# Performance work log

Measured on AMD Instinct MI355X. Metric: run time of the kernel, lower is better.

The kernel has to match this reference:

```python
import jax, jax.numpy as jnp
import numpy as np

B, NQ, NM, NHR, D, H, FF = 16, 100, 5440, 4096, 256, 8, 2048

def _ln(x, w, b):
    m = x.mean(-1, keepdims=True)
    v = ((x - m) ** 2).mean(-1, keepdims=True)
    return (x - m) * jax.lax.rsqrt(v + 1e-5) * w + b

def setup_inputs():
    key = jax.random.key(0)
    ks = iter(jax.random.split(key, 32))
    def rn(shape, s=1.0):
        return jax.random.normal(next(ks), shape, jnp.float32) * s
    return {
        'tgt': rn((B, NQ, D)),
        'memory': rn((B, NM, D)),
        'memory_hr': rn((B, NHR, D)),
        'prior_attn_bias': rn((B, NQ, NM)),
        'query_pos': rn((B, NQ, D)),
        'ln_cross_w': jnp.ones((D,)), 'ln_cross_b': jnp.zeros((D,)),
        'q_w': rn((D, D), 0.02), 'q_b': jnp.zeros((D,)),
        'k_w': rn((D, D), 0.02), 'k_b': jnp.zeros((D,)),
        'v_w': rn((D, D), 0.02), 'v_b': jnp.zeros((D,)),
        'out_w': rn((D, D), 0.02), 'out_b': jnp.zeros((D,)),
        'ln_self_w': jnp.ones((D,)), 'ln_self_b': jnp.zeros((D,)),
        'sa_in_w': rn((3 * D, D), 0.02), 'sa_in_b': jnp.zeros((3 * D,)),
        'sa_out_w': rn((D, D), 0.02), 'sa_out_b': jnp.zeros((D,)),
        'ln_ffn_w': jnp.ones((D,)), 'ln_ffn_b': jnp.zeros((D,)),
        'lin1_w': rn((FF, D), 0.02), 'lin1_b': jnp.zeros((FF,)),
        'lin2_w': rn((D, FF), 0.02), 'lin2_b': jnp.zeros((D,)),
        'me_w': rn((D, D), 0.02), 'me_b': jnp.zeros((D,)),
    }

def reference(tgt, memory, memory_hr, prior_attn_bias, query_pos,
              ln_cross_w, ln_cross_b, q_w, q_b, k_w, k_b, v_w, v_b,
              out_w, out_b, ln_self_w, ln_self_b, sa_in_w, sa_in_b,
              sa_out_w, sa_out_b, ln_ffn_w, ln_ffn_b, lin1_w, lin1_b,
              lin2_w, lin2_b, me_w, me_b):
    b, nq, d = tgt.shape
    nm = memory.shape[1]
    h = H
    dh = d // h
    scale = dh ** -0.5
    # ---- cross-attention with additive prior bias (eval mode: dropout = id) ----
    x = _ln(tgt, ln_cross_w, ln_cross_b)
    q = ((x + query_pos) @ q_w.T + q_b).reshape(b, nq, h, dh)
    k = (memory @ k_w.T + k_b).reshape(b, nm, h, dh)
    v = (memory @ v_w.T + v_b).reshape(b, nm, h, dh)
    attn = jnp.einsum('bqhd,bmhd->bhqm', q, k) * scale + prior_attn_bias[:, None]  # [b,h,nq,nm]
    a = jax.nn.softmax(attn, axis=-1)
    o = jnp.einsum('bhqm,bmhd->bqhd', a, v).reshape(b, nq, d)
    tgt = tgt + (o @ out_w.T + out_b)
    # ---- self-attention (torch nn.MultiheadAttention, batch_first, eval) ----
    z = _ln(tgt, ln_self_w, ln_self_b)
    zq = z + query_pos
    qs = (zq @ sa_in_w[:d].T + sa_in_b[:d]).reshape(b, nq, h, dh)
    ks = (zq @ sa_in_w[d:2 * d].T + sa_in_b[d:2 * d]).reshape(b, nq, h, dh)
    vs = (z @ sa_in_w[2 * d:].T + sa_in_b[2 * d:]).reshape(b, nq, h, dh)
    sattn = jax.nn.softmax(jnp.einsum('bqhd,bmhd->bhqm', qs, ks) * scale, axis=-1)
    so = jnp.einsum('bhqm,bmhd->bqhd', sattn, vs).reshape(b, nq, d)
    tgt = tgt + (so @ sa_out_w.T + sa_out_b)
    # ---- FFN ----
    y = _ln(tgt, ln_ffn_w, ln_ffn_b)
    y = jax.nn.gelu(y @ lin1_w.T + lin1_b, approximate=False) @ lin2_w.T + lin2_b
    tgt = tgt + y
    # ---- mask branch ----
    mask_logits = jnp.einsum('bqd,bmd->bqm', tgt @ me_w.T + me_b, memory_hr)
    return (tgt, mask_logits)
```

## Files before the change

kernel.cpp:

```cpp
#include <hip/hip_runtime.h>

typedef unsigned short u16;
typedef unsigned int u32;
typedef __bf16 bf16x8 __attribute__((ext_vector_type(8)));
typedef float f32x4 __attribute__((ext_vector_type(4)));
typedef float f32x16 __attribute__((ext_vector_type(16)));

#define NCH 17
#define NSTEP 10

__device__ __forceinline__ u16 f2b(float f) {
  u32 u = __float_as_uint(f);
  u32 r = (u + 0x7fffu + ((u >> 16) & 1u)) >> 16;
  return (u16)r;
}
__device__ __forceinline__ float b2f(u16 h) {
  return __uint_as_float(((u32)h) << 16);
}
__device__ __forceinline__ bf16x8 zero8() {
  union { uint4 u; bf16x8 v; } z; z.u = make_uint4(0u, 0u, 0u, 0u); return z.v;
}
__device__ __forceinline__ u32 cvtpk(float lo, float hi) {
  u32 r;
  asm("v_cvt_pk_bf16_f32 %0, %1, %2" : "=v"(r) : "v"(lo), "v"(hi));
  return r;
}

struct Seg { const float* in; u16* out; int n4; };
struct PrepArgs {
  Seg seg[7];
  const float *k_w, *v_w, *k_b, *v_b, *pbias;
  u16 *Wf;
  uint4 *biasT5;
  float *kvB;
};

__global__ __launch_bounds__(256)
void prep_kernel(PrepArgs a)
{
  __shared__ float S[100][34];
  const int bx = blockIdx.x, tid = threadIdx.x;
  if (bx < 1472) {
    int bxr = bx;
#pragma unroll
    for (int k = 0; k < 7; ++k) {
      const int nb = a.seg[k].n4 >> 8;
      if (bxr < nb) {
        const int i = bxr * 256 + tid;
        const float4 f = *(const float4*)(a.seg[k].in + (size_t)i * 4);
        uint2 pk; pk.x = cvtpk(f.x, f.y); pk.y = cvtpk(f.z, f.w);
        *(uint2*)(a.seg[k].out + (size_t)i * 4) = pk;
        return;
      }
      bxr -= nb;
    }
    return;
  } else if (bx < 1536) {
    const int i = bx - 1472, gI = i >> 3, ks = i & 7;
    const int nt = tid >> 6, lane = tid & 63, lr = lane & 15, g = lane >> 4;
    const float* src = (gI < 4 ? a.k_w + (size_t)(gI * 64 + nt * 16 + lr) * 256
                               : a.v_w + (size_t)((gI - 4) * 64 + nt * 16 + lr) * 256)
                       + ks * 32 + g * 8;
    const float4 f0 = *(const float4*)src;
    const float4 f1 = *(const float4*)(src + 4);
    uint4 pk;
    pk.x = cvtpk(f0.x, f0.y); pk.y = cvtpk(f0.z, f0.w);
    pk.z = cvtpk(f1.x, f1.y); pk.w = cvtpk(f1.z, f1.w);
    *(uint4*)(a.Wf + (size_t)((gI * 8 + ks) * 4 + nt) * 512 + lane * 8) = pk;
  } else if (bx < 1538) {
    const int i = (bx - 1536) * 256 + tid;
    a.kvB[i] = (i < 256) ? a.k_b[i] : a.v_b[i - 256];
  } else {
    const int bt = bx - 1538;
    const int b = bt / 170, sg = bt - b * 170;
    const int m0 = sg * 32;
    for (int idx = tid; idx < 800; idx += 256) {
      const int q = idx >> 3, seg = idx & 7;
      const float4 v = *(const float4*)(a.pbias + (size_t)(b * 100 + q) * 5440 + m0 + seg * 4);
      S[q][seg * 4 + 0] = v.x; S[q][seg * 4 + 1] = v.y;
      S[q][seg * 4 + 2] = v.z; S[q][seg * 4 + 3] = v.w;
    }
    __syncthreads();
#pragma unroll
    for (int pass = 0; pass < 2; ++pass) {
      const int idx = pass * 256 + tid;
      const int qb = idx >> 7, r2 = idx & 127;
      const int half = r2 >> 6, lane = r2 & 63;
      const int q = qb * 32 + (lane & 31), hh = lane >> 5;
      u16 hv[8];
#pragma unroll
      for (int i = 0; i < 8; ++i) {
        const int reg = half * 8 + i;
        const int m = (reg & 3) + 8 * (reg >> 2) + 4 * hh;
        hv[i] = (q < 100) ? f2b(S[q][m]) : (u16)0;
      }
      uint4 pk;
      pk.x = (u32)hv[0] | ((u32)hv[1] << 16);
      pk.y = (u32)hv[2] | ((u32)hv[3] << 16);
      pk.z = (u32)hv[4] | ((u32)hv[5] << 16);
      pk.w = (u32)hv[6] | ((u32)hv[7] << 16);
      a.biasT5[((size_t)(bt * 4 + qb)) * 128 + half * 64 + lane] = pk;
    }
  }
}

template<int ROWS>
__device__ __forceinline__ void ln_stage(const float* __restrict__ x, int row0,
    const float* __restrict__ w, const float* __restrict__ b,
    const float* __restrict__ pos, u16* As)
{
  const int tid = threadIdx.x, lane = tid & 63, wid = tid >> 6;
  const float4 wv = *(const float4*)(w + lane * 4);
  const float4 bv = *(const float4*)(b + lane * 4);
#pragma unroll
  for (int rr = 0; rr < ROWS / 4; ++rr) {
    const int rl = wid * (ROWS / 4) + rr;
    const size_t o = (size_t)(row0 + rl) * 256 + lane * 4;
    const float4 v = *(const float4*)(x + o);
    float s = v.x + v.y + v.z + v.w;
#pragma unroll
    for (int m = 1; m < 64; m <<= 1) s += __shfl_xor(s, m);
    const float mean = s * (1.f / 256.f);
    const float d0 = v.x - mean, d1 = v.y - mean, d2 = v.z - mean, d3 = v.w - mean;
    float ss = d0 * d0 + d1 * d1 + d2 * d2 + d3 * d3;
#pragma unroll
    for (int m = 1; m < 64; m <<= 1) ss += __shfl_xor(ss, m);
    const float rs = rsqrtf(ss * (1.f / 256.f) + 1e-5f);
    float y0 = d0 * rs * wv.x + bv.x;
    float y1 = d1 * rs * wv.y + bv.y;
    float y2 = d2 * rs * wv.z + bv.z;
    float y3 = d3 * rs * wv.w + bv.w;
    if (pos) {
      const float4 pv = *(const float4*)(pos + o);
      y0 += pv.x; y1 += pv.y; y2 += pv.z; y3 += pv.w;
    }
    uint2 pk; pk.x = cvtpk(y0, y1); pk.y = cvtpk(y2, y3);
    const int byte = (rl * 512 + lane * 8) ^ ((rl & 7) << 4);
    *(uint2*)((char*)As + byte) = pk;
  }
}

__device__ __forceinline__ void gemm16x128(const u16* As, const u16* __restrict__ W,
                                           u16 (*Ws)[40], f32x4 acc[2])
{
  const int tid = threadIdx.x, lane = tid & 63, wid = tid >> 6;
  const int g = lane >> 4, lr = lane & 15;
  for (int k0 = 0; k0 < 256; k0 += 32) {
    for (int cid = tid; cid < 512; cid += 256) {
      const int r = cid >> 2, cg = (cid & 3) * 8;
      *(uint4*)&Ws[r][cg] = *(const uint4*)(W + (size_t)r * 256 + k0 + cg);
    }
    __syncthreads();
    const int abyte = (lr * 512 + k0 * 2 + g * 16) ^ ((lr & 7) << 4);
    const bf16x8 af = *(const bf16x8*)((const char*)As + abyte);
#pragma unroll
    for (int nt = 0; nt < 2; ++nt) {
      const bf16x8 bfr = *(const bf16x8*)&Ws[wid * 32 + nt * 16 + lr][g * 8];
      acc[nt] = __builtin_amdgcn_mfma_f32_16x16x32_bf16(af, bfr, acc[nt], 0, 0, 0);
    }
    __syncthreads();
  }
}

__global__ __launch_bounds__(256)
void qproj_kernel(const float* __restrict__ x, const float* __restrict__ lnw,
                  const float* __restrict__ lnb, const float* __restrict__ pos,
                  const u16* __restrict__ W, const float* __restrict__ bias,
                  u16* __restrict__ out, float scale)
{
  __shared__ u16 As[16 * 256];
  __shared__ u16 Ws[128][40];
  const int tid = threadIdx.x, lane = tid & 63, wid = tid >> 6;
  const int g = lane >> 4, lr = lane & 15;
  const int row0 = blockIdx.x * 16, n0 = blockIdx.y * 128;
  ln_stage<16>(x, row0, lnw, lnb, pos, As);
  f32x4 acc[2] = {};
  gemm16x128(As, W + (size_t)n0 * 256, Ws, acc);
#pragma unroll
  for (int nt = 0; nt < 2; ++nt) {
    const int col = n0 + wid * 32 + nt * 16 + lr;
    const float bv = bias[col];
#pragma unroll
    for (int r = 0; r < 4; ++r) {
      const int row = row0 + g * 4 + r;
      out[(size_t)row * 256 + col] = f2b((acc[nt][r] + bv) * scale);
    }
  }
}

__global__ __launch_bounds__(256)
void sain_kernel(const float* __restrict__ x, const float* __restrict__ lnw,
                 const float* __restrict__ lnb, const float* __restrict__ pos,
                 const u16* __restrict__ W, const float* __restrict__ bias,
                 float* __restrict__ qkb, float* __restrict__ vsb)
{
  __shared__ u16 As[16 * 256];
  __shared__ u16 Ws[128][40];
  const int tid = threadIdx.x, lane = tid & 63, wid = tid >> 6;
  const int g = lane >> 4, lr = lane & 15;
  const int row0 = blockIdx.x * 16, y = blockIdx.y;
  ln_stage<16>(x, row0, lnw, lnb, (y < 4) ? pos : nullptr, As);
  f32x4 acc[2] = {};
  gemm16x128(As, W + (size_t)y * 128 * 256, Ws, acc);
#pragma unroll
  for (int nt = 0; nt < 2; ++nt) {
    const int cl = wid * 32 + nt * 16 + lr;
    const float bv = bias[y * 128 + cl];
#pragma unroll
    for (int r = 0; r < 4; ++r) {
      const int row = row0 + g * 4 + r;
      const float v = acc[nt][r] + bv;
      if (y < 4) qkb[(size_t)row * 512 + y * 128 + cl] = v;
      else       vsb[(size_t)row * 256 + (y - 4) * 128 + cl] = v;
    }
  }
}

__global__ __launch_bounds__(256)
void ffn1_kernel(const float* __restrict__ x, const float* __restrict__ lnw,
                 const float* __restrict__ lnb, const u16* __restrict__ W,
                 const float* __restrict__ bias, u16* __restrict__ out)
{
  __shared__ u16 As[64 * 256];
  __shared__ u16 Ws[256][40];
  const int tid = threadIdx.x, lane = tid & 63, wid = tid >> 6;
  const int g = lane >> 4, lr = lane & 15;
  const int row0 = blockIdx.x * 64, n0 = blockIdx.y * 256;
  ln_stage<64>(x, row0, lnw, lnb, nullptr, As);
  f32x4 acc[16] = {};
  for (int k0 = 0; k0 < 256; k0 += 32) {
    for (int cid = tid; cid < 1024; cid += 256) {
      const int r = cid >> 2, cg = (cid & 3) * 8;
      *(uint4*)&Ws[r][cg] = *(const uint4*)(W + (size_t)(n0 + r) * 256 + k0 + cg);
    }
    __syncthreads();
    const int arow = wid * 16 + lr;
    const int abyte = (arow * 512 + k0 * 2 + g * 16) ^ ((arow & 7) << 4);
    const bf16x8 af = *(const bf16x8*)((const char*)As + abyte);
#pragma unroll
    for (int nt = 0; nt < 16; ++nt) {
      const bf16x8 bfr = *(const bf16x8*)&Ws[nt * 16 + lr][g * 8];
      acc[nt] = __builtin_amdgcn_mfma_f32_16x16x32_bf16(af, bfr, acc[nt], 0, 0, 0);
    }
    __syncthreads();
  }
#pragma unroll
  for (int nt = 0; nt < 16; ++nt) {
    const int col = n0 + nt * 16 + lr;
    const float bv = bias[col];
#pragma unroll
    for (int r = 0; r < 4; ++r) {
      const int row = row0 + wid * 16 + g * 4 + r;
      float v = acc[nt][r] + bv;
      v = 0.5f * v * (1.f + erff(v * 0.70710678118654752f));
      out[(size_t)row * 2048 + col] = f2b(v);
    }
  }
}

template<int BM, int BN, int WM, int WN, int GELU_, int RES_, int OF32, int OBF>
__global__ __launch_bounds__(256)
void gemm_kernel(const u16* __restrict__ Ap, const u16* __restrict__ W,
                 const float* __restrict__ bias, const float* __restrict__ res,
                 float* __restrict__ Cf, u16* __restrict__ Cb,
                 int M, int N, int K, float scale)
{
  constexpr int WROWS = BM / WM;
  constexpr int WCOLS = BN / WN;
  constexpr int MT = WROWS / 16;
  constexpr int NT = WCOLS / 16;
  static_assert(WM * WN == 4, "4 waves");
  __shared__ u16 As[BM][40];
  __shared__ u16 Ws[BN][40];
  const int tid = threadIdx.x, lane = tid & 63, wid = tid >> 6;
  const int g = lane >> 4, lr = lane & 15;
  const int m0 = blockIdx.x * BM, n0 = blockIdx.y * BN;
  const int wm = wid / WN, wn = wid % WN;
  f32x4 acc[MT][NT] = {};
  for (int k0 = 0; k0 < K; k0 += 32) {
    for (int cid = tid; cid < BM * 4; cid += 256) {
      int r = cid >> 2, cg = (cid & 3) * 8;
      *(uint4*)&As[r][cg] = *(const uint4*)(Ap + (size_t)(m0 + r) * K + k0 + cg);
    }
    for (int cid = tid; cid < BN * 4; cid += 256) {
      int r = cid >> 2, cg = (cid & 3) * 8;
      *(uint4*)&Ws[r][cg] = *(const uint4*)(W + (size_t)(n0 + r) * K + k0 + cg);
    }
    __syncthreads();
    bf16x8 af[MT], bfr[NT];
#pragma unroll
    for (int mt = 0; mt < MT; ++mt) af[mt] = *(const bf16x8*)&As[wm * WROWS + mt * 16 + lr][g * 8];
#pragma unroll
    for (int nt = 0; nt < NT; ++nt) bfr[nt] = *(const bf16x8*)&Ws[wn * WCOLS + nt * 16 + lr][g * 8];
#pragma unroll
    for (int mt = 0; mt < MT; ++mt)
#pragma unroll
      for (int nt = 0; nt < NT; ++nt)
        acc[mt][nt] = __builtin_amdgcn_mfma_f32_16x16x32_bf16(af[mt], bfr[nt], acc[mt][nt], 0, 0, 0);
    __syncthreads();
  }
#pragma unroll
  for (int mt = 0; mt < MT; ++mt)
#pragma unroll
    for (int nt = 0; nt < NT; ++nt) {
      const int col = n0 + wn * WCOLS + nt * 16 + lr;
      const float bv = bias[col];
#pragma unroll
      for (int r = 0; r < 4; ++r) {
        const int row = m0 + wm * WROWS + mt * 16 + g * 4 + r;
        float v = (acc[mt][nt][r] + bv) * scale;
        if constexpr (GELU_) v = 0.5f * v * (1.f + erff(v * 0.70710678118654752f));
        if constexpr (RES_) v += res[(size_t)row * N + col];
        if constexpr (OF32) Cf[(size_t)row * N + col] = v;
        if constexpr (OBF) Cb[(size_t)row * N + col] = f2b(v);
      }
    }
}

__global__ __launch_bounds__(512, 4)
void kv_gemm_kernel(const float* __restrict__ A, const u16* __restrict__ Wf,
                    const float* __restrict__ biasKV,
                    u16* __restrict__ Kb, u16* __restrict__ Vt)
{
  __shared__ u16 As[64 * 256];
  __shared__ u16 Vs[256 * 64];
  const int tid = threadIdx.x, lane = tid & 63, wid = tid >> 6;
  const int g = lane >> 4, lr = lane & 15;
  const int bidx = blockIdx.x / 85, t = blockIdx.x - bidx * 85;
  const int row0 = blockIdx.x * 64;

  for (int ch = tid; ch < 2048; ch += 512) {
    const int r = ch >> 5, c8 = (ch & 31) * 8;
    const float* ap = A + (size_t)(row0 + r) * 256 + c8;
    const float4 f0 = *(const float4*)ap;
    const float4 f1 = *(const float4*)(ap + 4);
    uint4 pk;
    pk.x = cvtpk(f0.x, f0.y);
    pk.y = cvtpk(f0.z, f0.w);
    pk.z = cvtpk(f1.x, f1.y);
    pk.w = cvtpk(f1.z, f1.w);
    const int byte = r * 512 + c8 * 2;
    *(uint4*)((char*)As + (byte ^ ((r & 7) << 4))) = pk;
  }
  __syncthreads();

  const u16* wbase = Wf + (size_t)wid * 8 * 4 * 512 + lane * 8;
  f32x4 acc[4][4] = {};
#pragma unroll 2
  for (int ks = 0; ks < 8; ++ks) {
    bf16x8 bfv[4], af[4];
#pragma unroll
    for (int nt = 0; nt < 4; ++nt)
      bfv[nt] = *(const bf16x8*)(wbase + (ks * 4 + nt) * 512);
#pragma unroll
    for (int mt = 0; mt < 4; ++mt) {
      const int r = mt * 16 + lr;
      const int byte = r * 512 + ks * 64 + g * 16;
      af[mt] = *(const bf16x8*)((const char*)As + (byte ^ ((r & 7) << 4)));
    }
#pragma unroll
    for (int mt = 0; mt < 4; ++mt)
#pragma unroll
      for (int nt = 0; nt < 4; ++nt)
        acc[mt][nt] = __builtin_amdgcn_mfma_f32_16x16x32_bf16(af[mt], bfv[nt], acc[mt][nt], 0, 0, 0);
  }

  const int isV = wid >> 2;
  if (isV) {
#pragma unroll
    for (int nt = 0; nt < 4; ++nt) {
      const int col = (wid - 4) * 64 + nt * 16 + lr;
      const float bv = biasKV[256 + col];
#pragma unroll
      for (int mt = 0; mt < 4; ++mt) {
        const int slot = (mt >> 1) * 32 + 16 * (mt & 1) + 8 * (g & 1) + 4 * (g >> 1);
#pragma unroll
        for (int r = 0; r < 4; r += 2) {
          const u32 val = cvtpk(acc[mt][nt][r] + bv, acc[mt][nt][r + 1] + bv);
          const int byte = (col * 128 + (slot + r) * 2) ^ ((col & 7) << 4);
          *(u32*)((char*)Vs + byte) = val;
        }
      }
    }
  }
  __syncthreads();

  if (!isV) {
#pragma unroll
    for (int nt = 0; nt < 4; ++nt) {
      const int col = wid * 64 + nt * 16 + lr;
      const float bv = biasKV[col];
#pragma unroll
      for (int mt = 0; mt < 4; ++mt)
#pragma unroll
        for (int r = 0; r < 4; r += 2) {
          const u32 pk = cvtpk(acc[mt][nt][r] + bv, acc[mt][nt][r + 1] + bv);
          const int rowA = mt * 16 + g * 4 + r;
          const int rowB = rowA + 1;
          *(u16*)((char*)As + ((rowA * 512 + col * 2) ^ ((rowA & 7) << 4))) = (u16)pk;
          *(u16*)((char*)As + ((rowB * 512 + col * 2) ^ ((rowB & 7) << 4))) = (u16)(pk >> 16);
        }
    }
  } else {
    const size_t vbase = (size_t)bidx * 256 * 5440 + (size_t)t * 64;
    const int t2 = tid - 256;
#pragma unroll
    for (int p = 0; p < 8; ++p) {
      const int idx = p * 256 + t2;
      const int col = idx >> 3, chunk = idx & 7;
      const int lbyte = col * 128 + ((chunk * 16) ^ ((col & 7) << 4));
      const uint4 v = *(const uint4*)((const char*)Vs + lbyte);
      *(uint4*)(Vt + vbase + (size_t)col * 5440 + chunk * 8) = v;
    }
  }
  __syncthreads();
#pragma unroll
  for (int p = 0; p < 4; ++p) {
    const int idx = p * 512 + tid;
    const int row = idx >> 5, c16 = idx & 31;
    const int lbyte = row * 512 + ((c16 * 16) ^ ((row & 7) << 4));
    const uint4 v = *(const uint4*)((const char*)As + lbyte);
    *(uint4*)(Kb + (size_t)(row0 + row) * 256 + c16 * 8) = v;
  }
}

__global__ __launch_bounds__(256, 3)
void cross_attn_kernel(const u16* __restrict__ Q, const u16* __restrict__ Kb,
                       const u16* __restrict__ Vt, const uint4* __restrict__ biasT5,
                       u32* __restrict__ Opp, float* __restrict__ ML)
{
  const int tid = threadIdx.x, lane = tid & 63, wid = tid >> 6;
  const int ql = lane & 31, hh = lane >> 5;
  const int b = blockIdx.y, c = blockIdx.x;
  const int head = blockIdx.z * 4 + wid;
  const int m_base = c * (5440 / NCH);

  bf16x8 qf[4][2];
#pragma unroll
  for (int qb = 0; qb < 4; ++qb) {
    const int q = qb * 32 + ql;
#pragma unroll
    for (int hf = 0; hf < 2; ++hf)
      qf[qb][hf] = (q < 100)
        ? *(const bf16x8*)&Q[(size_t)(b * 100 + q) * 256 + head * 32 + hf * 16 + hh * 8]
        : zero8();
  }
  float M[4], L[4];
  f32x16 O[4];
#pragma unroll
  for (int qb = 0; qb < 4; ++qb) {
    M[qb] = -1e30f; L[qb] = 0.f;
#pragma unroll
    for (int i = 0; i < 16; ++i) O[qb][i] = 0.f;
  }

  for (int s = 0; s < NSTEP; ++s) {
    const int m0 = m_base + s * 32;
    const u16* kp = &Kb[(size_t)(b * 5440 + m0 + ql) * 256 + head * 32 + hh * 8];
    const bf16x8 kf0 = *(const bf16x8*)kp;
    const bf16x8 kf1 = *(const bf16x8*)(kp + 16);
    const u16* vp = &Vt[((size_t)(b * 8 + head) * 32 + ql) * 5440 + m0 + hh * 8];
    const bf16x8 vf0 = *(const bf16x8*)vp;
    const bf16x8 vf1 = *(const bf16x8*)(vp + 16);
    const uint4* bb = biasT5 + ((size_t)(b * 170 + c * NSTEP + s) * 4) * 128 + lane;
#pragma unroll
    for (int qb = 0; qb < 4; ++qb) {
      const uint4 b0 = bb[qb * 128];
      const uint4 b1 = bb[qb * 128 + 64];
      f32x16 Sv = {};
      __builtin_amdgcn_s_setprio(1);
      Sv = __builtin_amdgcn_mfma_f32_32x32x16_bf16(kf0, qf[qb][0], Sv, 0, 0, 0);
      Sv = __builtin_amdgcn_mfma_f32_32x32x16_bf16(kf1, qf[qb][1], Sv, 0, 0, 0);
      __builtin_amdgcn_s_setprio(0);
      const u32 bw[8] = {b0.x, b0.y, b0.z, b0.w, b1.x, b1.y, b1.z, b1.w};
#pragma unroll
      for (int i = 0; i < 8; ++i) {
        Sv[2 * i]     += b2f((u16)bw[i]);
        Sv[2 * i + 1] += b2f((u16)(bw[i] >> 16));
      }
      float t8[8];
#pragma unroll
      for (int i = 0; i < 8; ++i) t8[i] = fmaxf(Sv[2 * i], Sv[2 * i + 1]);
      float t4a = fmaxf(fmaxf(t8[0], t8[1]), fmaxf(t8[2], t8[3]));
      float t4b = fmaxf(fmaxf(t8[4], t8[5]), fmaxf(t8[6], t8[7]));
      float mx = fmaxf(t4a, t4b);
      mx = fmaxf(mx, __shfl_xor(mx, 32));
      const float newM = fmaxf(M[qb], mx);
      const float al = __expf(M[qb] - newM);
      M[qb] = newM;
      float p[16];
#pragma unroll
      for (int i = 0; i < 16; ++i) p[i] = __expf(Sv[i] - newM);
      float s8[8];
#pragma unroll
      for (int i = 0; i < 8; ++i) s8[i] = p[2 * i] + p[2 * i + 1];
      const float sum = ((s8[0] + s8[1]) + (s8[2] + s8[3])) + ((s8[4] + s8[5]) + (s8[6] + s8[7]));
      L[qb] = L[qb] * al + sum;
#pragma unroll
      for (int i = 0; i < 16; ++i) O[qb][i] *= al;
      union { uint4 u; bf16x8 v; } pb0, pb1;
      pb0.u.x = cvtpk(p[0], p[1]);   pb0.u.y = cvtpk(p[2], p[3]);
      pb0.u.z = cvtpk(p[4], p[5]);   pb0.u.w = cvtpk(p[6], p[7]);
      pb1.u.x = cvtpk(p[8], p[9]);   pb1.u.y = cvtpk(p[10], p[11]);
      pb1.u.z = cvtpk(p[12], p[13]); pb1.u.w = cvtpk(p[14], p[15]);
      __builtin_amdgcn_s_setprio(1);
      O[qb] = __builtin_amdgcn_mfma_f32_32x32x16_bf16(vf0, pb0.v, O[qb], 0, 0, 0);
      O[qb] = __builtin_amdgcn_mfma_f32_32x32x16_bf16(vf1, pb1.v, O[qb], 0, 0, 0);
      __builtin_amdgcn_s_setprio(0);
    }
  }
  const int bh = b * 8 + head;
#pragma unroll
  for (int qb = 0; qb < 4; ++qb) {
    const int q = qb * 32 + ql;
    const float Lt = L[qb] + __shfl_xor(L[qb], 32);
    if (q < 100) {
      const size_t rb = (size_t)(bh * NCH + c) * 128 + q;
#pragma unroll
      for (int i = 0; i < 8; ++i)
        Opp[rb * 16 + hh * 8 + i] = cvtpk(O[qb][2 * i], O[qb][2 * i + 1]);
      if (hh == 0) { ML[rb * 2] = M[qb]; ML[rb * 2 + 1] = Lt; }
    }
  }
}

__global__ __launch_bounds__(256)
void reduce_attn_kernel(const u32* __restrict__ Opp, const float* __restrict__ ML,
                        u16* __restrict__ outb)
{
  const int row = blockIdx.x;
  const int b = row / 100, q = row % 100;
  const int h = threadIdx.x >> 5, d = threadIdx.x & 31;
  const int bh = b * 8 + h;
  const int reg = (d & 3) + 4 * (d >> 3);
  const int slot = ((d >> 2) & 1) * 8 + (reg >> 1);
  const int half = reg & 1;
  float gm = -1e30f;
  for (int c = 0; c < NCH; ++c) gm = fmaxf(gm, ML[((size_t)(bh * NCH + c) * 128 + q) * 2]);
  float l = 0.f, o = 0.f;
  for (int c = 0; c < NCH; ++c) {
    const size_t rb = (size_t)(bh * NCH + c) * 128 + q;
    const float w = __expf(ML[rb * 2] - gm);
    l += ML[rb * 2 + 1] * w;
    const u32 pv = Opp[rb * 16 + slot];
    o += b2f((u16)(half ? (pv >> 16) : pv)) * w;
  }
  outb[(size_t)row * 256 + h * 32 + d] = f2b(o / l);
}

__global__ __launch_bounds__(128)
void self_attn_kernel(const float* __restrict__ qk, const float* __restrict__ vs,
                      u16* __restrict__ so)
{
  __shared__ u16 kk[100][36];
  __shared__ u16 vv[100][36];
  __shared__ float S[100][101];
  const int b = blockIdx.x >> 3, h = blockIdx.x & 7;
  const int t = threadIdx.x;
  for (int e = t; e < 3200; e += 128) {
    const int r = e >> 5, cq = e & 31;
    kk[r][cq] = f2b(qk[(size_t)(b * 100 + r) * 512 + 256 + h * 32 + cq]);
    vv[r][cq] = f2b(vs[(size_t)(b * 100 + r) * 256 + h * 32 + cq]);
  }
  __syncthreads();
  if (t < 100) {
    float qr_[32];
#pragma unroll
    for (int cq = 0; cq < 32; ++cq) qr_[cq] = qk[(size_t)(b * 100 + t) * 512 + h * 32 + cq];
    for (int m = 0; m < 100; ++m) {
      float dp = 0.f;
#pragma unroll
      for (int cq = 0; cq < 32; ++cq) dp += qr_[cq] * b2f(kk[m][cq]);
      S[t][m] = dp * 0.17677669529663687f;
    }
    float mx = -1e30f;
    for (int m = 0; m < 100; ++m) mx = fmaxf(mx, S[t][m]);
    float sum = 0.f;
    for (int m = 0; m < 100; ++m) { const float p = __expf(S[t][m] - mx); S[t][m] = p; sum += p; }
    const float inv = 1.f / sum;
    float o[32];
#pragma unroll
    for (int cq = 0; cq < 32; ++cq) o[cq] = 0.f;
    for (int m = 0; m < 100; ++m) {
      const float p = S[t][m];
#pragma unroll
      for (int cq = 0; cq < 32; ++cq) o[cq] += p * b2f(vv[m][cq]);
    }
#pragma unroll
    for (int cq = 0; cq < 32; ++cq)
      so[(size_t)(b * 100 + t) * 256 + h * 32 + cq] = f2b(o[cq] * inv);
  }
}

__global__ __launch_bounds__(256)
void mask_gemm_kernel(const u16* __restrict__ tm, const float* __restrict__ hr,
                      float* __restrict__ out)
{
  __shared__ u16 As[112][40];
  __shared__ u16 Bs[64][40];
  const int tid = threadIdx.x, lane = tid & 63, wid = tid >> 6;
  const int g = lane >> 4, lr = lane & 15;
  const int b = blockIdx.y, n0 = blockIdx.x * 64;
  f32x4 acc[7] = {};
  for (int k0 = 0; k0 < 256; k0 += 32) {
    for (int cid = tid; cid < 448; cid += 256) {
      const int r = cid >> 2, cg = (cid & 3) * 8;
      uint4 val = {0u, 0u, 0u, 0u};
      if (r < 100) val = *(const uint4*)&tm[(size_t)(b * 100 + r) * 256 + k0 + cg];
      *(uint4*)&As[r][cg] = val;
    }
    {
      const int r = tid >> 2, cg = (tid & 3) * 8;
      const float* hp = hr + (size_t)(b * 4096 + n0 + r) * 256 + k0 + cg;
      float4 f0 = *(const float4*)hp;
      float4 f1 = *(const float4*)(hp + 4);
      uint4 pk;
      pk.x = cvtpk(f0.x, f0.y); pk.y = cvtpk(f0.z, f0.w);
      pk.z = cvtpk(f1.x, f1.y); pk.w = cvtpk(f1.z, f1.w);
      *(uint4*)&Bs[r][cg] = pk;
    }
    __syncthreads();
    const bf16x8 bfr = *(const bf16x8*)&Bs[wid * 16 + lr][g * 8];
#pragma unroll
    for (int mt = 0; mt < 7; ++mt) {
      const bf16x8 af = *(const bf16x8*)&As[mt * 16 + lr][g * 8];
      acc[mt] = __builtin_amdgcn_mfma_f32_16x16x32_bf16(af, bfr, acc[mt], 0, 0, 0);
    }
    __syncthreads();
  }
#pragma unroll
  for (int mt = 0; mt < 7; ++mt)
#pragma unroll
    for (int r = 0; r < 4; ++r) {
      const int qr = mt * 16 + g * 4 + r;
      if (qr < 100)
        out[(size_t)(b * 100 + qr) * 4096 + n0 + wid * 16 + lr] = acc[mt][r];
    }
}

extern "C" void kernel_launch(void* const* d_in, const int* in_sizes, int n_in,
                              void* d_out, int out_size, void* d_ws, size_t ws_size,
                              hipStream_t stream)
{
  (void)in_sizes; (void)n_in; (void)out_size; (void)ws_size;
  const float* tgt      = (const float*)d_in[0];
  const float* memory   = (const float*)d_in[1];
  const float* memhr    = (const float*)d_in[2];
  const float* pbias    = (const float*)d_in[3];
  const float* qpos     = (const float*)d_in[4];
  const float* lncw     = (const float*)d_in[5];
  const float* lncb     = (const float*)d_in[6];
  const float* q_w      = (const float*)d_in[7];
  const float* q_b      = (const float*)d_in[8];
  const float* k_w      = (const float*)d_in[9];
  const float* k_b      = (const float*)d_in[10];
  const float* v_w      = (const float*)d_in[11];
  const float* v_b      = (const float*)d_in[12];
  const float* out_w    = (const float*)d_in[13];
  const float* out_b    = (const float*)d_in[14];
  const float* lnsw     = (const float*)d_in[15];
  const float* lnsb     = (const float*)d_in[16];
  const float* sa_in_w  = (const float*)d_in[17];
  const float* sa_in_b  = (const float*)d_in[18];
  const float* sa_out_w = (const float*)d_in[19];
  const float* sa_out_b = (const float*)d_in[20];
  const float* lnfw     = (const float*)d_in[21];
  const float* lnfb     = (const float*)d_in[22];
  const float* l1w      = (const float*)d_in[23];
  const float* l1b      = (const float*)d_in[24];
  const float* l2w      = (const float*)d_in[25];
  const float* l2b      = (const float*)d_in[26];
  const float* me_w     = (const float*)d_in[27];
  const float* me_b     = (const float*)d_in[28];
  float* outf = (float*)d_out;

  char* ws = (char*)d_ws;
  size_t off = 0;
  auto alloc = [&](size_t bytes) -> void* {
    void* p = ws + off;
    off = (off + bytes + 255) & ~(size_t)255;
    return p;
  };
  u16*   Wf    = (u16*)alloc((size_t)131072 * 2);
  u16*   qW    = (u16*)alloc((size_t)65536 * 2);
  u16*   outW  = (u16*)alloc((size_t)65536 * 2);
  u16*   saW   = (u16*)alloc((size_t)196608 * 2);
  u16*   saoW  = (u16*)alloc((size_t)65536 * 2);
  u16*   l1W   = (u16*)alloc((size_t)524288 * 2);
  u16*   l2W   = (u16*)alloc((size_t)524288 * 2);
  u16*   meW   = (u16*)alloc((size_t)65536 * 2);
  float* kvB   = (float*)alloc((size_t)512 * 4);
  uint4* biasT5= (uint4*)alloc((size_t)16 * 170 * 4 * 128 * 16);
  u16*   Qb    = (u16*)alloc((size_t)409600 * 2);
  u16*   Kb    = (u16*)alloc((size_t)22282240 * 2);
  u16*   Vt    = (u16*)alloc((size_t)22282240 * 2);
  u32*   Opp   = (u32*)alloc((size_t)(128 * NCH * 128 * 16) * 4);
  float* MLp   = (float*)alloc((size_t)(128 * NCH * 128 * 2) * 4);
  u16*   attno = (u16*)alloc((size_t)409600 * 2);
  float* tgt1  = (float*)alloc((size_t)409600 * 4);
  float* qkb   = (float*)alloc((size_t)819200 * 4);
  float* vsb   = (float*)alloc((size_t)409600 * 4);
  u16*   sob   = (u16*)alloc((size_t)409600 * 2);
  float* tgt2  = (float*)alloc((size_t)409600 * 4);
  u16*   hb    = (u16*)alloc((size_t)3276800 * 2);
  u16*   t3b   = (u16*)alloc((size_t)409600 * 2);
  u16*   tmb   = (u16*)alloc((size_t)409600 * 2);

  const float SCALE = 0.17677669529663687f;

  PrepArgs pa;
  pa.seg[0] = {q_w,      qW,   16384};
  pa.seg[1] = {out_w,    outW, 16384};
  pa.seg[2] = {sa_in_w,  saW,  49152};
  pa.seg[3] = {sa_out_w, saoW, 16384};
  pa.seg[4] = {l1w,      l1W,  131072};
  pa.seg[5] = {l2w,      l2W,  131072};
  pa.seg[6] = {me_w,     meW,  16384};
  pa.k_w = k_w; pa.v_w = v_w; pa.k_b = k_b; pa.v_b = v_b; pa.pbias = pbias;
  pa.Wf = Wf; pa.biasT5 = biasT5; pa.kvB = kvB;
  prep_kernel<<<4258, 256, 0, stream>>>(pa);

  qproj_kernel<<<dim3(100, 2), 256, 0, stream>>>(tgt, lncw, lncb, qpos, qW, q_b, Qb, SCALE);
  kv_gemm_kernel<<<dim3(1360), 512, 0, stream>>>(memory, Wf, kvB, Kb, Vt);
  cross_attn_kernel<<<dim3(NCH, 16, 2), 256, 0, stream>>>(Qb, Kb, Vt, biasT5, Opp, MLp);
  reduce_attn_kernel<<<1600, 256, 0, stream>>>(Opp, MLp, attno);
  gemm_kernel<16, 128, 1, 4, 0, 1, 1, 0><<<dim3(100, 2), 256, 0, stream>>>(
      attno, outW, out_b, tgt, tgt1, nullptr, 1600, 256, 256, 1.f);

  sain_kernel<<<dim3(100, 6), 256, 0, stream>>>(tgt1, lnsw, lnsb, qpos, saW, sa_in_b, qkb, vsb);
  self_attn_kernel<<<128, 128, 0, stream>>>(qkb, vsb, sob);
  gemm_kernel<16, 128, 1, 4, 0, 1, 1, 0><<<dim3(100, 2), 256, 0, stream>>>(
      sob, saoW, sa_out_b, tgt1, tgt2, nullptr, 1600, 256, 256, 1.f);

  ffn1_kernel<<<dim3(25, 8), 256, 0, stream>>>(tgt2, lnfw, lnfb, l1W, l1b, hb);
  gemm_kernel<16, 128, 1, 4, 0, 1, 1, 1><<<dim3(100, 2), 256, 0, stream>>>(
      hb, l2W, l2b, tgt2, outf, t3b, 1600, 256, 2048, 1.f);

  gemm_kernel<16, 128, 1, 4, 0, 0, 0, 1><<<dim3(100, 2), 256, 0, stream>>>(
      t3b, meW, me_b, nullptr, nullptr, tmb, 1600, 256, 256, 1.f);
  mask_gemm_kernel<<<dim3(64, 16), 256, 0, stream>>>(tmb, memhr, outf + 409600);
}
```

Measured before the change: 326.5 us.

## Remap cross-attention waves to query blocks of one head

Each wave of the cross-attention kernel now owns a single 32-query block of one head, instead of one head with all four query blocks. The grid grows from 2 to 8 in z, so there are four times as many blocks and each thread keeps far fewer registers (one O accumulator instead of four). Launch bounds rise to 4 blocks per SIMD-level occupancy target. The cost is that K and V fragments are now loaded once per query block rather than shared across four, which multiplies global/L2 traffic for K/V, and the wave holding queries 96-127 does mostly padding work.

Result: faster. 312.7 us (-4.2%).

```diff
diff --git a/kernel.cpp b/kernel.cpp
--- a/kernel.cpp
+++ b/kernel.cpp
@@ -424,35 +424,28 @@
   }
 }
 
-__global__ __launch_bounds__(256, 3)
+__global__ __launch_bounds__(256, 4)
 void cross_attn_kernel(const u16* __restrict__ Q, const u16* __restrict__ Kb,
                        const u16* __restrict__ Vt, const uint4* __restrict__ biasT5,
                        u32* __restrict__ Opp, float* __restrict__ ML)
 {
-  const int tid = threadIdx.x, lane = tid & 63, wid = tid >> 6;
+  const int tid = threadIdx.x, lane = tid & 63, qb = tid >> 6;
   const int ql = lane & 31, hh = lane >> 5;
   const int b = blockIdx.y, c = blockIdx.x;
-  const int head = blockIdx.z * 4 + wid;
+  const int head = blockIdx.z;
   const int m_base = c * (5440 / NCH);
-
-  bf16x8 qf[4][2];
-#pragma unroll
-  for (int qb = 0; qb < 4; ++qb) {
-    const int q = qb * 32 + ql;
-#pragma unroll
-    for (int hf = 0; hf < 2; ++hf)
-      qf[qb][hf] = (q < 100)
-        ? *(const bf16x8*)&Q[(size_t)(b * 100 + q) * 256 + head * 32 + hf * 16 + hh * 8]
-        : zero8();
-  }
-  float M[4], L[4];
-  f32x16 O[4];
-#pragma unroll
-  for (int qb = 0; qb < 4; ++qb) {
-    M[qb] = -1e30f; L[qb] = 0.f;
-#pragma unroll
-    for (int i = 0; i < 16; ++i) O[qb][i] = 0.f;
-  }
+  const int q = qb * 32 + ql;
+
+  bf16x8 qf0 = zero8(), qf1 = zero8();
+  if (q < 100) {
+    const u16* qp = &Q[(size_t)(b * 100 + q) * 256 + head * 32 + hh * 8];
+    qf0 = *(const bf16x8*)qp;
+    qf1 = *(const bf16x8*)(qp + 16);
+  }
+  float M = -1e30f, L = 0.f;
+  f32x16 O;
+#pragma unroll
+  for (int i = 0; i < 16; ++i) O[i] = 0.f;
 
   for (int s = 0; s < NSTEP; ++s) {
     const int m0 = m_base + s * 32;
@@ -462,65 +455,58 @@
     const u16* vp = &Vt[((size_t)(b * 8 + head) * 32 + ql) * 5440 + m0 + hh * 8];
     const bf16x8 vf0 = *(const bf16x8*)vp;
     const bf16x8 vf1 = *(const bf16x8*)(vp + 16);
-    const uint4* bb = biasT5 + ((size_t)(b * 170 + c * NSTEP + s) * 4) * 128 + lane;
-#pragma unroll
-    for (int qb = 0; qb < 4; ++qb) {
-      const uint4 b0 = bb[qb * 128];
-      const uint4 b1 = bb[qb * 128 + 64];
-      f32x16 Sv = {};
-      __builtin_amdgcn_s_setprio(1);
-      Sv = __builtin_amdgcn_mfma_f32_32x32x16_bf16(kf0, qf[qb][0], Sv, 0, 0, 0);
-      Sv = __builtin_amdgcn_mfma_f32_32x32x16_bf16(kf1, qf[qb][1], Sv, 0, 0, 0);
-      __builtin_amdgcn_s_setprio(0);
-      const u32 bw[8] = {b0.x, b0.y, b0.z, b0.w, b1.x, b1.y, b1.z, b1.w};
-#pragma unroll
-      for (int i = 0; i < 8; ++i) {
-        Sv[2 * i]     += b2f((u16)bw[i]);
-        Sv[2 * i + 1] += b2f((u16)(bw[i] >> 16));
-      }
-      float t8[8];
-#pragma unroll
-      for (int i = 0; i < 8; ++i) t8[i] = fmaxf(Sv[2 * i], Sv[2 * i + 1]);
-      float t4a = fmaxf(fmaxf(t8[0], t8[1]), fmaxf(t8[2], t8[3]));
-      float t4b = fmaxf(fmaxf(t8[4], t8[5]), fmaxf(t8[6], t8[7]));
-      float mx = fmaxf(t4a, t4b);
-      mx = fmaxf(mx, __shfl_xor(mx, 32));
-      const float newM = fmaxf(M[qb], mx);
-      const float al = __expf(M[qb] - newM);
-      M[qb] = newM;
-      float p[16];
-#pragma unroll
-      for (int i = 0; i < 16; ++i) p[i] = __expf(Sv[i] - newM);
-      float s8[8];
-#pragma unroll
-      for (int i = 0; i < 8; ++i) s8[i] = p[2 * i] + p[2 * i + 1];
-      const float sum = ((s8[0] + s8[1]) + (s8[2] + s8[3])) + ((s8[4] + s8[5]) + (s8[6] + s8[7]));
-      L[qb] = L[qb] * al + sum;
-#pragma unroll
-      for (int i = 0; i < 16; ++i) O[qb][i] *= al;
-      union { uint4 u; bf16x8 v; } pb0, pb1;
-      pb0.u.x = cvtpk(p[0], p[1]);   pb0.u.y = cvtpk(p[2], p[3]);
-      pb0.u.z = cvtpk(p[4], p[5]);   pb0.u.w = cvtpk(p[6], p[7]);
-      pb1.u.x = cvtpk(p[8], p[9]);   pb1.u.y = cvtpk(p[10], p[11]);
-      pb1.u.z = cvtpk(p[12], p[13]); pb1.u.w = cvtpk(p[14], p[15]);
-      __builtin_amdgcn_s_setprio(1);
-      O[qb] = __builtin_amdgcn_mfma_f32_32x32x16_bf16(vf0, pb0.v, O[qb], 0, 0, 0);
-      O[qb] = __builtin_amdgcn_mfma_f32_32x32x16_bf16(vf1, pb1.v, O[qb], 0, 0, 0);
-      __builtin_amdgcn_s_setprio(0);
-    }
+    const uint4* bb = biasT5 + ((size_t)((b * 170 + c * NSTEP + s) * 4 + qb)) * 128 + lane;
+    const uint4 b0 = bb[0];
+    const uint4 b1 = bb[64];
+    f32x16 Sv = {};
+    __builtin_amdgcn_s_setprio(1);
+    Sv = __builtin_amdgcn_mfma_f32_32x32x16_bf16(kf0, qf0, Sv, 0, 0, 0);
+    Sv = __builtin_amdgcn_mfma_f32_32x32x16_bf16(kf1, qf1, Sv, 0, 0, 0);
+    __builtin_amdgcn_s_setprio(0);
+    const u32 bw[8] = {b0.x, b0.y, b0.z, b0.w, b1.x, b1.y, b1.z, b1.w};
+#pragma unroll
+    for (int i = 0; i < 8; ++i) {
+      Sv[2 * i]     += b2f((u16)bw[i]);
+      Sv[2 * i + 1] += b2f((u16)(bw[i] >> 16));
+    }
+    float t8[8];
+#pragma unroll
+    for (int i = 0; i < 8; ++i) t8[i] = fmaxf(Sv[2 * i], Sv[2 * i + 1]);
+    float t4a = fmaxf(fmaxf(t8[0], t8[1]), fmaxf(t8[2], t8[3]));
+    float t4b = fmaxf(fmaxf(t8[4], t8[5]), fmaxf(t8[6], t8[7]));
+    float mx = fmaxf(t4a, t4b);
+    mx = fmaxf(mx, __shfl_xor(mx, 32));
+    const float newM = fmaxf(M, mx);
+    const float al = __expf(M - newM);
+    M = newM;
+    float p[16];
+#pragma unroll
+    for (int i = 0; i < 16; ++i) p[i] = __expf(Sv[i] - newM);
+    float s8[8];
+#pragma unroll
+    for (int i = 0; i < 8; ++i) s8[i] = p[2 * i] + p[2 * i + 1];
+    const float sum = ((s8[0] + s8[1]) + (s8[2] + s8[3])) + ((s8[4] + s8[5]) + (s8[6] + s8[7]));
+    L = L * al + sum;
+#pragma unroll
+    for (int i = 0; i < 16; ++i) O[i] *= al;
+    union { uint4 u; bf16x8 v; } pb0, pb1;
+    pb0.u.x = cvtpk(p[0], p[1]);   pb0.u.y = cvtpk(p[2], p[3]);
+    pb0.u.z = cvtpk(p[4], p[5]);   pb0.u.w = cvtpk(p[6], p[7]);
+    pb1.u.x = cvtpk(p[8], p[9]);   pb1.u.y = cvtpk(p[10], p[11]);
+    pb1.u.z = cvtpk(p[12], p[13]); pb1.u.w = cvtpk(p[14], p[15]);
+    __builtin_amdgcn_s_setprio(1);
+    O = __builtin_amdgcn_mfma_f32_32x32x16_bf16(vf0, pb0.v, O, 0, 0, 0);
+    O = __builtin_amdgcn_mfma_f32_32x32x16_bf16(vf1, pb1.v, O, 0, 0, 0);
+    __builtin_amdgcn_s_setprio(0);
   }
   const int bh = b * 8 + head;
-#pragma unroll
-  for (int qb = 0; qb < 4; ++qb) {
-    const int q = qb * 32 + ql;
-    const float Lt = L[qb] + __shfl_xor(L[qb], 32);
-    if (q < 100) {
-      const size_t rb = (size_t)(bh * NCH + c) * 128 + q;
-#pragma unroll
-      for (int i = 0; i < 8; ++i)
-        Opp[rb * 16 + hh * 8 + i] = cvtpk(O[qb][2 * i], O[qb][2 * i + 1]);
-      if (hh == 0) { ML[rb * 2] = M[qb]; ML[rb * 2 + 1] = Lt; }
-    }
+  const float Lt = L + __shfl_xor(L, 32);
+  if (q < 100) {
+    const size_t rb = (size_t)(bh * NCH + c) * 128 + q;
+#pragma unroll
+    for (int i = 0; i < 8; ++i)
+      Opp[rb * 16 + hh * 8 + i] = cvtpk(O[2 * i], O[2 * i + 1]);
+    if (hh == 0) { ML[rb * 2] = M; ML[rb * 2 + 1] = Lt; }
   }
 }
 
@@ -722,7 +708,7 @@
 
   qproj_kernel<<<dim3(100, 2), 256, 0, stream>>>(tgt, lncw, lncb, qpos, qW, q_b, Qb, SCALE);
   kv_gemm_kernel<<<dim3(1360), 512, 0, stream>>>(memory, Wf, kvB, Kb, Vt);
-  cross_attn_kernel<<<dim3(NCH, 16, 2), 256, 0, stream>>>(Qb, Kb, Vt, biasT5, Opp, MLp);
+  cross_attn_kernel<<<dim3(NCH, 16, 8), 256, 0, stream>>>(Qb, Kb, Vt, biasT5, Opp, MLp);
   reduce_attn_kernel<<<1600, 256, 0, stream>>>(Opp, MLp, attno);
   gemm_kernel<16, 128, 1, 4, 0, 1, 1, 0><<<dim3(100, 2), 256, 0, stream>>>(
       attno, outW, out_b, tgt, tgt1, nullptr, 1600, 256, 256, 1.f);
```
